# Kernel tuning notes

Measured on AMD Instinct MI355X. Metric: run time of the kernel, lower is better.

The kernel has to match this reference:

```python
import jax, jax.numpy as jnp
import numpy as np

N = 100000
E = 1_600_000
IN = 128
HID = 32
HEADS = 4
OUT = 2
NEG_SLOPE = 0.2  # PyG GATv2Conv default negative_slope


def setup_inputs() -> dict:
    key = jax.random.key(0)
    ks = jax.random.split(key, 18)
    g = lambda k, shape, fan: jax.random.normal(k, shape, dtype=jnp.float32) / np.sqrt(fan)
    return {
        "x": jax.random.normal(ks[0], (N, IN), dtype=jnp.float32),
        "edge_index": jax.random.randint(ks[1], (2, E), 0, N, dtype=jnp.int32),
        # conv1: GATv2Conv(IN, HID, heads=HEADS)
        "W1l": g(ks[2], (IN, HEADS * HID), IN),
        "b1l": jnp.zeros((HEADS * HID,), jnp.float32),
        "W1r": g(ks[3], (IN, HEADS * HID), IN),
        "b1r": jnp.zeros((HEADS * HID,), jnp.float32),
        "att1": g(ks[4], (HEADS, HID), HID),
        "bias1": jnp.zeros((HEADS * HID,), jnp.float32),
        # conv2: GATv2Conv(HEADS*HID, HID, heads=1)
        "W2l": g(ks[5], (HEADS * HID, HID), HEADS * HID),
        "b2l": jnp.zeros((HID,), jnp.float32),
        "W2r": g(ks[6], (HEADS * HID, HID), HEADS * HID),
        "b2r": jnp.zeros((HID,), jnp.float32),
        "att2": g(ks[7], (1, HID), HID),
        "bias2": jnp.zeros((HID,), jnp.float32),
        # final linear
        "Wlin": g(ks[8], (HID, OUT), HID),
        "blin": jnp.zeros((OUT,), jnp.float32),
    }


def _gatv2(x, src, dst, Wl, bl, Wr, br, att, bias, heads, ch):
    n = x.shape[0]
    xl = (x @ Wl + bl).reshape(n, heads, ch)  # source transform
    xr = (x @ Wr + br).reshape(n, heads, ch)  # target transform
    # GATv2 edge score: a^T LeakyReLU(xl_j + xr_i)
    e = jax.nn.leaky_relu(xl[src] + xr[dst], NEG_SLOPE)      # [E, H, C]
    score = jnp.einsum('ehc,hc->eh', e, att)                  # [E, H]
    # segment softmax over edges sharing a destination node
    m = jax.ops.segment_max(score, dst, num_segments=n)
    ex = jnp.exp(score - m[dst])
    denom = jax.ops.segment_sum(ex, dst, num_segments=n)
    alpha = ex / denom[dst]                                   # [E, H]
    out = jax.ops.segment_sum(alpha[..., None] * xl[src], dst, num_segments=n)
    return out.reshape(n, heads * ch) + bias


def reference(x, edge_index, W1l, b1l, W1r, b1r, att1, bias1,
              W2l, b2l, W2r, b2r, att2, bias2, Wlin, blin):
    # add self-loops (PyG GATv2Conv default add_self_loops=True)
    loop = jnp.arange(N, dtype=edge_index.dtype)
    src = jnp.concatenate([edge_index[0], loop])
    dst = jnp.concatenate([edge_index[1], loop])

    h = _gatv2(x, src, dst, W1l, b1l, W1r, b1r, att1, bias1, HEADS, HID)
    h = jax.nn.elu(h)
    # dropout is inactive in eval mode
    h = _gatv2(h, src, dst, W2l, b2l, W2r, b2r, att2, bias2, 1, HID)
    h = jax.nn.elu(h)
    return h @ Wlin + blin  # [N, OUT]
```

## Files before the change

### kernel.cpp

```cpp
#include <hip/hip_runtime.h>
#include <hip/hip_fp16.h>
#include <math.h>

#define N_NODES 100000
#define E_EDGES 1600000
#define ETOT (E_EDGES + N_NODES)
#define NEG 0.2f
#define NB 782
#define NREP 4
#define SEG 704
#define BCAP (NREP * SEG)
#define CHUNK 4096
#define NCHB ((E_EDGES + CHUNK - 1) / CHUNK)
#define GEMM1_BLOCKS ((N_NODES + 63) / 64)

typedef _Float16 half8 __attribute__((ext_vector_type(8)));
typedef _Float16 half4v __attribute__((ext_vector_type(4)));
typedef _Float16 half2v __attribute__((ext_vector_type(2)));
typedef float floatx4 __attribute__((ext_vector_type(4)));

union H8I {
  half8 v;
  _Float16 e[8];
  int i[4];
};

__device__ __forceinline__ float elu(float v) { return v > 0.f ? v : (__expf(v) - 1.f); }

__device__ __forceinline__ float score8(half8 a, half8 r, half8 av) {
  half8 t = a + r;
  t = __builtin_elementwise_max(t, t * (_Float16)NEG);
  half8 s8 = t * av;
  half4v s4 = __builtin_shufflevector(s8, s8, 0, 1, 2, 3) +
              __builtin_shufflevector(s8, s8, 4, 5, 6, 7);
  half2v s2 = __builtin_shufflevector(s4, s4, 0, 1) +
              __builtin_shufflevector(s4, s4, 2, 3);
  return (float)s2[0] + (float)s2[1];
}

__global__ __launch_bounds__(256) void fusedA_kernel(
    const int* __restrict__ ei, unsigned* __restrict__ cursor,
    unsigned* __restrict__ bins,
    const float* __restrict__ W1l, const float* __restrict__ W1r,
    const float* __restrict__ b1l, const float* __restrict__ b1r,
    const float* __restrict__ W2l, const float* __restrict__ W2r,
    const float* __restrict__ b2l, const float* __restrict__ b2r,
    const float* __restrict__ att1, const float* __restrict__ att2,
    _Float16* __restrict__ Bperm, _Float16* __restrict__ B2perm,
    float* __restrict__ biascat, float* __restrict__ bias2cat,
    _Float16* __restrict__ att1h, _Float16* __restrict__ att2h) {
  int t = threadIdx.x;
  if (blockIdx.x < NCHB) {
    __shared__ unsigned cnt[NB];
    __shared__ unsigned base[NB];
    int rep = blockIdx.x & (NREP - 1);
    for (int b = t; b < NB; b += 256) cnt[b] = 0;
    __syncthreads();
    int e0 = blockIdx.x * CHUNK;
    int dstr[CHUNK / 256];
#pragma unroll
    for (int i = 0; i < CHUNK / 256; i++) {
      int e = e0 + i * 256 + t;
      int dst = 0;
      if (e < E_EDGES) {
        dst = ei[E_EDGES + e];
        atomicAdd(&cnt[dst >> 7], 1u);
      }
      dstr[i] = dst;
    }
    __syncthreads();
    for (int b = t; b < NB; b += 256) {
      unsigned c = cnt[b];
      base[b] = c ? atomicAdd(&cursor[rep * NB + b], c) : 0u;
      cnt[b] = 0;
    }
    __syncthreads();
#pragma unroll
    for (int i = 0; i < CHUNK / 256; i++) {
      int e = e0 + i * 256 + t;
      if (e < E_EDGES) {
        int dst = dstr[i];
        int src = ei[e];
        int b = dst >> 7;
        unsigned off = atomicAdd(&cnt[b], 1u);
        bins[(size_t)b * BCAP + rep * SEG + base[b] + off] =
            ((unsigned)(dst & 127) << 17) | (unsigned)src;
      }
    }
  } else {
    int pb = blockIdx.x - NCHB;
    int gt = pb * 256 + t;
    int gstr = 20 * 256;
    for (int e = gt; e < 4096; e += gstr) {
      int nt = e >> 8, kt = (e >> 6) & 3, lane = e & 63;
      int n = nt * 16 + (lane & 15);
      int kb = kt * 32 + (lane >> 4) * 8;
#pragma unroll
      for (int j = 0; j < 8; j++) {
        int k = kb + j;
        float val = (n < 128) ? W1l[k * 128 + n] : W1r[k * 128 + (n - 128)];
        Bperm[(size_t)e * 8 + j] = (_Float16)val;
      }
    }
    for (int e = gt; e < 1024; e += gstr) {
      int nt = e >> 8, kt = (e >> 6) & 3, lane = e & 63;
      int n = nt * 16 + (lane & 15);
      int kb = kt * 32 + (lane >> 4) * 8;
#pragma unroll
      for (int j = 0; j < 8; j++) {
        int k = kb + j;
        float val = (n < 32) ? W2l[k * 32 + n] : W2r[k * 32 + (n - 32)];
        B2perm[(size_t)e * 8 + j] = (_Float16)val;
      }
    }
    if (pb == 0) {
      biascat[t] = (t < 128) ? b1l[t] : b1r[t - 128];
      if (t < 64) bias2cat[t] = (t < 32) ? b2l[t] : b2r[t - 32];
      if (t < 128) att1h[t] = (_Float16)att1[t];
      if (t < 32) att2h[t] = (_Float16)att2[t];
    }
  }
}

__global__ __launch_bounds__(1024) void scan_buckets(const unsigned* __restrict__ cursor,
                                                     unsigned* __restrict__ bucket_base,
                                                     unsigned* __restrict__ rowptr) {
  __shared__ unsigned s[1024];
  int t = threadIdx.x;
  unsigned v = 0;
  if (t < NB) {
#pragma unroll
    for (int r = 0; r < NREP; r++) v += cursor[r * NB + t];
    int nib = N_NODES - (t << 7);
    v += (nib > 128) ? 128u : (unsigned)nib;
  }
  s[t] = v;
  __syncthreads();
  for (int off = 1; off < 1024; off <<= 1) {
    unsigned a = (t >= off) ? s[t - off] : 0u;
    __syncthreads();
    s[t] += a;
    __syncthreads();
  }
  if (t < NB) bucket_base[t] = s[t] - v;
  if (t == 0) { bucket_base[NB] = ETOT; rowptr[N_NODES] = ETOT; }
}

__global__ __launch_bounds__(256) void fusedB_kernel(
    const unsigned* __restrict__ bins, const unsigned* __restrict__ cursor,
    const unsigned* __restrict__ bucket_base,
    unsigned* __restrict__ rowptr, int* __restrict__ csr_src,
    const float* __restrict__ x, const _Float16* __restrict__ Bperm,
    const float* __restrict__ biascat,
    __half* __restrict__ xlh, __half* __restrict__ xrh) {
  __shared__ __align__(16) char smem[64 * 256];
  int t = threadIdx.x;
  if (blockIdx.x < NB) {
    unsigned* cnt = (unsigned*)smem;
    unsigned* pref = cnt + 128;
    int b = blockIdx.x;
    int nib = N_NODES - (b << 7);
    if (nib > 128) nib = 128;
    unsigned bbase = bucket_base[b];
    unsigned crs[NREP];
#pragma unroll
    for (int r = 0; r < NREP; r++) crs[r] = cursor[r * NB + b];
    const unsigned* bp = bins + (size_t)b * BCAP;
    if (t < 128) cnt[t] = 0;
    __syncthreads();
#pragma unroll
    for (int r = 0; r < NREP; r++)
      for (unsigned i = t; i < crs[r]; i += 256)
        atomicAdd(&cnt[bp[r * SEG + i] >> 17], 1u);
    __syncthreads();
    if (t < 128) pref[t] = (t < nib) ? cnt[t] + 1u : 0u;
    __syncthreads();
    for (int off = 1; off < 128; off <<= 1) {
      unsigned a = (t >= off && t < 128) ? pref[t - off] : 0u;
      __syncthreads();
      if (t < 128) pref[t] += a;
      __syncthreads();
    }
    if (t < 128) {
      unsigned tot = (t < nib) ? cnt[t] + 1u : 0u;
      unsigned excl = pref[t] - tot;
      pref[t] = excl;
      if (t < nib) {
        int n = (b << 7) + t;
        rowptr[n] = bbase + excl;
        csr_src[bbase + excl] = n;
      }
      cnt[t] = 0;
    }
    __syncthreads();
#pragma unroll
    for (int r = 0; r < NREP; r++)
      for (unsigned i = t; i < crs[r]; i += 256) {
        unsigned en = bp[r * SEG + i];
        int j = (int)(en >> 17);
        unsigned off = atomicAdd(&cnt[j], 1u);
        csr_src[bbase + pref[j] + 1u + off] = (int)(en & 0x1FFFFu);
      }
  } else {
    int base = (blockIdx.x - NB) * 64;
    {
      int row = t >> 2, c4 = t & 3;
      int grow = base + row;
      const float* gp = x + (size_t)grow * 128 + c4 * 32;
#pragma unroll
      for (int j = 0; j < 4; j++) {
        half8 v = {};
        if (grow < N_NODES) {
          float4 f0 = *(const float4*)(gp + j * 8);
          float4 f1 = *(const float4*)(gp + j * 8 + 4);
          v[0] = (_Float16)f0.x; v[1] = (_Float16)f0.y;
          v[2] = (_Float16)f0.z; v[3] = (_Float16)f0.w;
          v[4] = (_Float16)f1.x; v[5] = (_Float16)f1.y;
          v[6] = (_Float16)f1.z; v[7] = (_Float16)f1.w;
        }
        int off = row * 256 + ((((c4 * 4 + j) * 16)) ^ ((row & 7) << 4));
        *(half8*)(smem + off) = v;
      }
    }
    int wid = t >> 6, lane = t & 63;
    half8 bf[4][4];
#pragma unroll
    for (int ntl = 0; ntl < 4; ntl++)
#pragma unroll
      for (int kt = 0; kt < 4; kt++) {
        int f = (wid * 4 + ntl) * 4 + kt;
        bf[ntl][kt] = *(const half8*)(Bperm + ((size_t)f * 64 + lane) * 8);
      }
    floatx4 acc[4][4] = {};
    __syncthreads();
#pragma unroll
    for (int kt = 0; kt < 4; kt++) {
      half8 a[4];
#pragma unroll
      for (int mt = 0; mt < 4; mt++) {
        int row = mt * 16 + (lane & 15);
        int kchunk = kt * 4 + (lane >> 4);
        int off = row * 256 + ((kchunk * 16) ^ ((row & 7) << 4));
        a[mt] = *(const half8*)(smem + off);
      }
#pragma unroll
      for (int mt = 0; mt < 4; mt++)
#pragma unroll
        for (int ntl = 0; ntl < 4; ntl++)
          acc[mt][ntl] = __builtin_amdgcn_mfma_f32_16x16x32_f16(a[mt], bf[ntl][kt],
                                                                acc[mt][ntl], 0, 0, 0);
    }
#pragma unroll
    for (int mt = 0; mt < 4; mt++) {
#pragma unroll
      for (int i = 0; i < 4; i++) {
        int row = base + mt * 16 + (lane >> 4) * 4 + i;
        if (row >= N_NODES) continue;
#pragma unroll
        for (int ntl = 0; ntl < 4; ntl++) {
          int col = wid * 64 + ntl * 16 + (lane & 15);
          float v = acc[mt][ntl][i] + biascat[col];
          if (col < 128) xlh[(size_t)row * 128 + col] = __float2half_rn(v);
          else xrh[(size_t)row * 128 + (col - 128)] = __float2half_rn(v);
        }
      }
    }
  }
}

__global__ __launch_bounds__(256) void gemm2_mfma(
    const __half* __restrict__ h1h, const _Float16* __restrict__ B2perm,
    const float* __restrict__ bias2cat,
    __half* __restrict__ xl2h, __half* __restrict__ xr2h) {
  __shared__ __align__(16) char smem[64 * 256];
  int t = threadIdx.x;
  int base = blockIdx.x * 64;
  {
    int row = t >> 2, c4 = t & 3;
    int grow = base + row;
    const char* gp = (const char*)(h1h + (size_t)grow * 128 + c4 * 32);
#pragma unroll
    for (int j = 0; j < 4; j++) {
      half8 v = {};
      if (grow < N_NODES) v = *(const half8*)(gp + j * 16);
      int off = row * 256 + ((((c4 * 4 + j) * 16)) ^ ((row & 7) << 4));
      *(half8*)(smem + off) = v;
    }
  }
  int wid = t >> 6, lane = t & 63;
  half8 bf[4];
#pragma unroll
  for (int kt = 0; kt < 4; kt++) {
    int f = wid * 4 + kt;
    bf[kt] = *(const half8*)(B2perm + ((size_t)f * 64 + lane) * 8);
  }
  floatx4 acc[4] = {};
  __syncthreads();
#pragma unroll
  for (int kt = 0; kt < 4; kt++) {
    half8 a[4];
#pragma unroll
    for (int mt = 0; mt < 4; mt++) {
      int row = mt * 16 + (lane & 15);
      int kchunk = kt * 4 + (lane >> 4);
      int off = row * 256 + ((kchunk * 16) ^ ((row & 7) << 4));
      a[mt] = *(const half8*)(smem + off);
    }
#pragma unroll
    for (int mt = 0; mt < 4; mt++)
      acc[mt] = __builtin_amdgcn_mfma_f32_16x16x32_f16(a[mt], bf[kt], acc[mt], 0, 0, 0);
  }
  int col = wid * 16 + (lane & 15);
  float bv = bias2cat[col];
#pragma unroll
  for (int mt = 0; mt < 4; mt++) {
#pragma unroll
    for (int i = 0; i < 4; i++) {
      int row = base + mt * 16 + (lane >> 4) * 4 + i;
      if (row >= N_NODES) continue;
      float v = acc[mt][i] + bv;
      if (col < 32) xl2h[(size_t)row * 32 + col] = __float2half_rn(v);
      else xr2h[(size_t)row * 32 + (col - 32)] = __float2half_rn(v);
    }
  }
}

__global__ __launch_bounds__(256) void l1_gather_kernel(
    const __half* __restrict__ xlh, const __half* __restrict__ xrh,
    const int* __restrict__ csr_src, const unsigned* __restrict__ rowptr,
    const _Float16* __restrict__ att1h, const float* __restrict__ bias,
    __half* __restrict__ h1h) {
  int wid = threadIdx.x >> 6;
  int lane = threadIdx.x & 63;
  int n = blockIdx.x * 4 + wid;
  if (n >= N_NODES) return;
  int g = lane >> 4;
  int q = lane & 15;
  int c0 = q * 8;
  half8 rv = *(const half8*)(xrh + (size_t)n * 128 + c0);
  half8 av = *(const half8*)(att1h + c0);
  unsigned beg = rowptr[n], end = rowptr[n + 1];
  unsigned deg = end - beg;
  unsigned niter = deg >> 2, rem = deg & 3;
  float d0 = 0.f, d1 = 0.f;
  H8I acc0, acc1;
  acc0.v = (half8){};
  acc1.v = (half8){};
  unsigned e = beg + g;
  unsigned i = 0;
  for (; i + 2 <= niter; i += 2, e += 8) {
    int s0 = csr_src[e];
    int s1 = csr_src[e + 4];
    H8I a0, a1;
    a0.v = *(const half8*)(xlh + (size_t)s0 * 128 + c0);
    a1.v = *(const half8*)(xlh + (size_t)s1 * 128 + c0);
    float v0 = score8(a0.v, rv, av);
    float v1 = score8(a1.v, rv, av);
    v0 += __shfl_xor(v0, 1);  v1 += __shfl_xor(v1, 1);
    v0 += __shfl_xor(v0, 2);  v1 += __shfl_xor(v1, 2);
    float p0 = __expf(v0 - 4.f);
    float p1 = __expf(v1 - 4.f);
    d0 += p0; d1 += p1;
    _Float16 ph0 = (_Float16)p0, ph1 = (_Float16)p1;
    half8 p80 = {ph0, ph0, ph0, ph0, ph0, ph0, ph0, ph0};
    half8 p81 = {ph1, ph1, ph1, ph1, ph1, ph1, ph1, ph1};
    acc0.v = p80 * a0.v + acc0.v;
    acc1.v = p81 * a1.v + acc1.v;
  }
  if (i < niter) {
    int s0 = csr_src[e];
    H8I a0;
    a0.v = *(const half8*)(xlh + (size_t)s0 * 128 + c0);
    float v0 = score8(a0.v, rv, av);
    v0 += __shfl_xor(v0, 1);
    v0 += __shfl_xor(v0, 2);
    float p0 = __expf(v0 - 4.f);
    d0 += p0;
    _Float16 ph0 = (_Float16)p0;
    half8 p80 = {ph0, ph0, ph0, ph0, ph0, ph0, ph0, ph0};
    acc0.v = p80 * a0.v + acc0.v;
    e += 4;
  }
  if (rem) {
    bool valid = (unsigned)g < rem;
    int s0 = csr_src[valid ? e : beg];
    H8I a0;
    a0.v = *(const half8*)(xlh + (size_t)s0 * 128 + c0);
    float v0 = score8(a0.v, rv, av);
    v0 += __shfl_xor(v0, 1);
    v0 += __shfl_xor(v0, 2);
    float p0 = valid ? __expf(v0 - 4.f) : 0.f;
    d0 += p0;
    _Float16 ph0 = (_Float16)p0;
    half8 p80 = {ph0, ph0, ph0, ph0, ph0, ph0, ph0, ph0};
    acc0.v = p80 * a0.v + acc0.v;
  }
  float d = d0 + d1;
  H8I acc;
  acc.v = acc0.v + acc1.v;
#pragma unroll
  for (int msk = 16; msk <= 32; msk <<= 1) {
    d += __shfl_xor(d, msk);
    H8I o;
#pragma unroll
    for (int k = 0; k < 4; k++) o.i[k] = __shfl_xor(acc.i[k], msk);
    acc.v = acc.v + o.v;
  }
  if (g == 0) {
    float inv = 1.f / d;
    H8I res;
#pragma unroll
    for (int j = 0; j < 8; j++)
      res.e[j] = (_Float16)elu((float)acc.e[j] * inv + bias[c0 + j]);
    *(half8*)(h1h + (size_t)n * 128 + c0) = res.v;
  }
}

__global__ __launch_bounds__(256) void l2_gather_kernel(
    const __half* __restrict__ xl2h, const __half* __restrict__ xr2h,
    const int* __restrict__ csr_src, const unsigned* __restrict__ rowptr,
    const _Float16* __restrict__ att2h, const float* __restrict__ bias,
    const float* __restrict__ Wlin, const float* __restrict__ blin,
    float* __restrict__ out) {
  int wid = threadIdx.x >> 6;
  int lane = threadIdx.x & 63;
  int n = blockIdx.x * 4 + wid;
  if (n >= N_NODES) return;
  int g = lane >> 2;
  int q = lane & 3;
  int c0 = q * 8;
  half8 rv = *(const half8*)(xr2h + (size_t)n * 32 + c0);
  half8 av = *(const half8*)(att2h + c0);
  unsigned beg = rowptr[n], end = rowptr[n + 1];
  unsigned deg = end - beg;
  unsigned nfull = deg >> 4, rem = deg & 15;
  float d = 0.f;
  H8I acc;
  acc.v = (half8){};
  unsigned e = beg + g;
  for (unsigned i = 0; i < nfull; i++, e += 16) {
    int s = csr_src[e];
    H8I a;
    a.v = *(const half8*)(xl2h + (size_t)s * 32 + c0);
    float v = score8(a.v, rv, av);
    v += __shfl_xor(v, 1);
    v += __shfl_xor(v, 2);
    float p = __expf(v - 4.f);
    d += p;
    _Float16 ph = (_Float16)p;
    half8 p8 = {ph, ph, ph, ph, ph, ph, ph, ph};
    acc.v = p8 * a.v + acc.v;
  }
  if (rem) {
    bool valid = (unsigned)g < rem;
    int s = csr_src[valid ? e : beg];
    H8I a;
    a.v = *(const half8*)(xl2h + (size_t)s * 32 + c0);
    float v = score8(a.v, rv, av);
    v += __shfl_xor(v, 1);
    v += __shfl_xor(v, 2);
    float p = valid ? __expf(v - 4.f) : 0.f;
    d += p;
    _Float16 ph = (_Float16)p;
    half8 p8 = {ph, ph, ph, ph, ph, ph, ph, ph};
    acc.v = p8 * a.v + acc.v;
  }
#pragma unroll
  for (int msk = 4; msk <= 32; msk <<= 1) {
    d += __shfl_xor(d, msk);
    H8I o;
#pragma unroll
    for (int k = 0; k < 4; k++) o.i[k] = __shfl_xor(acc.i[k], msk);
    acc.v = acc.v + o.v;
  }
  float inv = 1.f / d;
  float o0 = 0.f, o1 = 0.f;
#pragma unroll
  for (int j = 0; j < 8; j++) {
    float v = elu((float)acc.e[j] * inv + bias[c0 + j]);
    o0 = fmaf(v, Wlin[(c0 + j) * 2 + 0], o0);
    o1 = fmaf(v, Wlin[(c0 + j) * 2 + 1], o1);
  }
  o0 += __shfl_xor(o0, 1); o1 += __shfl_xor(o1, 1);
  o0 += __shfl_xor(o0, 2); o1 += __shfl_xor(o1, 2);
  if (lane == 0) {
    out[(size_t)n * 2 + 0] = o0 + blin[0];
    out[(size_t)n * 2 + 1] = o1 + blin[1];
  }
}

extern "C" void kernel_launch(void* const* d_in, const int* in_sizes, int n_in,
                              void* d_out, int out_size, void* d_ws, size_t ws_size,
                              hipStream_t stream) {
  const float* x     = (const float*)d_in[0];
  const int*   ei    = (const int*)d_in[1];
  const float* W1l   = (const float*)d_in[2];
  const float* b1l   = (const float*)d_in[3];
  const float* W1r   = (const float*)d_in[4];
  const float* b1r   = (const float*)d_in[5];
  const float* att1  = (const float*)d_in[6];
  const float* bias1 = (const float*)d_in[7];
  const float* W2l   = (const float*)d_in[8];
  const float* b2l   = (const float*)d_in[9];
  const float* W2r   = (const float*)d_in[10];
  const float* b2r   = (const float*)d_in[11];
  const float* att2  = (const float*)d_in[12];
  const float* bias2 = (const float*)d_in[13];
  const float* Wlin  = (const float*)d_in[14];
  const float* blin  = (const float*)d_in[15];
  float* out = (float*)d_out;

  __half* xl1h  = (__half*)d_ws;
  __half* xr1h  = xl1h + (size_t)N_NODES * 128;
  __half* h1h   = xr1h + (size_t)N_NODES * 128;
  __half* xl2h  = h1h + (size_t)N_NODES * 128;
  __half* xr2h  = xl2h + (size_t)N_NODES * 32;
  _Float16* Bperm  = (_Float16*)(xr2h + (size_t)N_NODES * 32);
  _Float16* B2perm = Bperm + 32768;
  _Float16* att1h  = B2perm + 8192;
  _Float16* att2h  = att1h + 128;
  float* biascat   = (float*)(att2h + 32);
  float* bias2cat  = biascat + 256;
  int* csr_src     = (int*)(bias2cat + 64);
  unsigned* rowptr = (unsigned*)(csr_src + (size_t)ETOT);
  unsigned* cursor = rowptr + (N_NODES + 1);
  unsigned* bucket_base = cursor + NREP * NB;
  unsigned* bins   = bucket_base + NB + 1;

  (void)hipMemsetAsync(cursor, 0, (size_t)NREP * NB * sizeof(unsigned), stream);
  fusedA_kernel<<<NCHB + 20, 256, 0, stream>>>(
      ei, cursor, bins, W1l, W1r, b1l, b1r, W2l, W2r, b2l, b2r, att1, att2,
      Bperm, B2perm, biascat, bias2cat, att1h, att2h);
  scan_buckets<<<1, 1024, 0, stream>>>(cursor, bucket_base, rowptr);
  fusedB_kernel<<<NB + GEMM1_BLOCKS, 256, 0, stream>>>(
      bins, cursor, bucket_base, rowptr, csr_src, x, Bperm, biascat, xl1h, xr1h);

  l1_gather_kernel<<<(N_NODES + 3) / 4, 256, 0, stream>>>(
      (const __half*)xl1h, (const __half*)xr1h, csr_src, rowptr, att1h, bias1, h1h);

  gemm2_mfma<<<GEMM1_BLOCKS, 256, 0, stream>>>(h1h, B2perm, bias2cat, xl2h, xr2h);
  l2_gather_kernel<<<(N_NODES + 3) / 4, 256, 0, stream>>>(
      xl2h, xr2h, csr_src, rowptr, att2h, bias2, Wlin, blin, out);
}
```

Baseline: 228.5 us.

## Move layer-1 GEMM into the binning kernel and split weight packing out

```diff
diff --git a/kernel.cpp b/kernel.cpp
--- a/kernel.cpp
+++ b/kernel.cpp
@@ -38,9 +38,7 @@
   return (float)s2[0] + (float)s2[1];
 }
 
-__global__ __launch_bounds__(256) void fusedA_kernel(
-    const int* __restrict__ ei, unsigned* __restrict__ cursor,
-    unsigned* __restrict__ bins,
+__global__ __launch_bounds__(256) void pack_w_kernel(
     const float* __restrict__ W1l, const float* __restrict__ W1r,
     const float* __restrict__ b1l, const float* __restrict__ b1r,
     const float* __restrict__ W2l, const float* __restrict__ W2r,
@@ -50,9 +48,49 @@
     float* __restrict__ biascat, float* __restrict__ bias2cat,
     _Float16* __restrict__ att1h, _Float16* __restrict__ att2h) {
   int t = threadIdx.x;
+  int gt = blockIdx.x * 256 + t;
+  int gstr = gridDim.x * 256;
+  for (int e = gt; e < 4096; e += gstr) {
+    int nt = e >> 8, kt = (e >> 6) & 3, lane = e & 63;
+    int n = nt * 16 + (lane & 15);
+    int kb = kt * 32 + (lane >> 4) * 8;
+#pragma unroll
+    for (int j = 0; j < 8; j++) {
+      int k = kb + j;
+      float val = (n < 128) ? W1l[k * 128 + n] : W1r[k * 128 + (n - 128)];
+      Bperm[(size_t)e * 8 + j] = (_Float16)val;
+    }
+  }
+  for (int e = gt; e < 1024; e += gstr) {
+    int nt = e >> 8, kt = (e >> 6) & 3, lane = e & 63;
+    int n = nt * 16 + (lane & 15);
+    int kb = kt * 32 + (lane >> 4) * 8;
+#pragma unroll
+    for (int j = 0; j < 8; j++) {
+      int k = kb + j;
+      float val = (n < 32) ? W2l[k * 32 + n] : W2r[k * 32 + (n - 32)];
+      B2perm[(size_t)e * 8 + j] = (_Float16)val;
+    }
+  }
+  if (blockIdx.x == 0) {
+    biascat[t] = (t < 128) ? b1l[t] : b1r[t - 128];
+    if (t < 64) bias2cat[t] = (t < 32) ? b2l[t] : b2r[t - 32];
+    if (t < 128) att1h[t] = (_Float16)att1[t];
+    if (t < 32) att2h[t] = (_Float16)att2[t];
+  }
+}
+
+__global__ __launch_bounds__(256) void fusedbin_kernel(
+    const int* __restrict__ ei, unsigned* __restrict__ cursor,
+    unsigned* __restrict__ bins,
+    const float* __restrict__ x, const _Float16* __restrict__ Bperm,
+    const float* __restrict__ biascat,
+    __half* __restrict__ xlh, __half* __restrict__ xrh) {
+  __shared__ __align__(16) char smem[64 * 256];
+  int t = threadIdx.x;
   if (blockIdx.x < NCHB) {
-    __shared__ unsigned cnt[NB];
-    __shared__ unsigned base[NB];
+    unsigned* cnt = (unsigned*)smem;
+    unsigned* base = cnt + NB;
     int rep = blockIdx.x & (NREP - 1);
     for (int b = t; b < NB; b += 256) cnt[b] = 0;
     __syncthreads();
@@ -88,121 +126,7 @@
       }
     }
   } else {
-    int pb = blockIdx.x - NCHB;
-    int gt = pb * 256 + t;
-    int gstr = 20 * 256;
-    for (int e = gt; e < 4096; e += gstr) {
-      int nt = e >> 8, kt = (e >> 6) & 3, lane = e & 63;
-      int n = nt * 16 + (lane & 15);
-      int kb = kt * 32 + (lane >> 4) * 8;
-#pragma unroll
-      for (int j = 0; j < 8; j++) {
-        int k = kb + j;
-        float val = (n < 128) ? W1l[k * 128 + n] : W1r[k * 128 + (n - 128)];
-        Bperm[(size_t)e * 8 + j] = (_Float16)val;
-      }
-    }
-    for (int e = gt; e < 1024; e += gstr) {
-      int nt = e >> 8, kt = (e >> 6) & 3, lane = e & 63;
-      int n = nt * 16 + (lane & 15);
-      int kb = kt * 32 + (lane >> 4) * 8;
-#pragma unroll
-      for (int j = 0; j < 8; j++) {
-        int k = kb + j;
-        float val = (n < 32) ? W2l[k * 32 + n] : W2r[k * 32 + (n - 32)];
-        B2perm[(size_t)e * 8 + j] = (_Float16)val;
-      }
-    }
-    if (pb == 0) {
-      biascat[t] = (t < 128) ? b1l[t] : b1r[t - 128];
-      if (t < 64) bias2cat[t] = (t < 32) ? b2l[t] : b2r[t - 32];
-      if (t < 128) att1h[t] = (_Float16)att1[t];
-      if (t < 32) att2h[t] = (_Float16)att2[t];
-    }
-  }
-}
-
-__global__ __launch_bounds__(1024) void scan_buckets(const unsigned* __restrict__ cursor,
-                                                     unsigned* __restrict__ bucket_base,
-                                                     unsigned* __restrict__ rowptr) {
-  __shared__ unsigned s[1024];
-  int t = threadIdx.x;
-  unsigned v = 0;
-  if (t < NB) {
-#pragma unroll
-    for (int r = 0; r < NREP; r++) v += cursor[r * NB + t];
-    int nib = N_NODES - (t << 7);
-    v += (nib > 128) ? 128u : (unsigned)nib;
-  }
-  s[t] = v;
-  __syncthreads();
-  for (int off = 1; off < 1024; off <<= 1) {
-    unsigned a = (t >= off) ? s[t - off] : 0u;
-    __syncthreads();
-    s[t] += a;
-    __syncthreads();
-  }
-  if (t < NB) bucket_base[t] = s[t] - v;
-  if (t == 0) { bucket_base[NB] = ETOT; rowptr[N_NODES] = ETOT; }
-}
-
-__global__ __launch_bounds__(256) void fusedB_kernel(
-    const unsigned* __restrict__ bins, const unsigned* __restrict__ cursor,
-    const unsigned* __restrict__ bucket_base,
-    unsigned* __restrict__ rowptr, int* __restrict__ csr_src,
-    const float* __restrict__ x, const _Float16* __restrict__ Bperm,
-    const float* __restrict__ biascat,
-    __half* __restrict__ xlh, __half* __restrict__ xrh) {
-  __shared__ __align__(16) char smem[64 * 256];
-  int t = threadIdx.x;
-  if (blockIdx.x < NB) {
-    unsigned* cnt = (unsigned*)smem;
-    unsigned* pref = cnt + 128;
-    int b = blockIdx.x;
-    int nib = N_NODES - (b << 7);
-    if (nib > 128) nib = 128;
-    unsigned bbase = bucket_base[b];
-    unsigned crs[NREP];
-#pragma unroll
-    for (int r = 0; r < NREP; r++) crs[r] = cursor[r * NB + b];
-    const unsigned* bp = bins + (size_t)b * BCAP;
-    if (t < 128) cnt[t] = 0;
-    __syncthreads();
-#pragma unroll
-    for (int r = 0; r < NREP; r++)
-      for (unsigned i = t; i < crs[r]; i += 256)
-        atomicAdd(&cnt[bp[r * SEG + i] >> 17], 1u);
-    __syncthreads();
-    if (t < 128) pref[t] = (t < nib) ? cnt[t] + 1u : 0u;
-    __syncthreads();
-    for (int off = 1; off < 128; off <<= 1) {
-      unsigned a = (t >= off && t < 128) ? pref[t - off] : 0u;
-      __syncthreads();
-      if (t < 128) pref[t] += a;
-      __syncthreads();
-    }
-    if (t < 128) {
-      unsigned tot = (t < nib) ? cnt[t] + 1u : 0u;
-      unsigned excl = pref[t] - tot;
-      pref[t] = excl;
-      if (t < nib) {
-        int n = (b << 7) + t;
-        rowptr[n] = bbase + excl;
-        csr_src[bbase + excl] = n;
-      }
-      cnt[t] = 0;
-    }
-    __syncthreads();
-#pragma unroll
-    for (int r = 0; r < NREP; r++)
-      for (unsigned i = t; i < crs[r]; i += 256) {
-        unsigned en = bp[r * SEG + i];
-        int j = (int)(en >> 17);
-        unsigned off = atomicAdd(&cnt[j], 1u);
-        csr_src[bbase + pref[j] + 1u + off] = (int)(en & 0x1FFFFu);
-      }
-  } else {
-    int base = (blockIdx.x - NB) * 64;
+    int base = (blockIdx.x - NCHB) * 64;
     {
       int row = t >> 2, c4 = t & 3;
       int grow = base + row;
@@ -266,6 +190,81 @@
       }
     }
   }
+}
+
+__global__ __launch_bounds__(1024) void scan_buckets(const unsigned* __restrict__ cursor,
+                                                     unsigned* __restrict__ bucket_base,
+                                                     unsigned* __restrict__ rowptr) {
+  __shared__ unsigned s[1024];
+  int t = threadIdx.x;
+  unsigned v = 0;
+  if (t < NB) {
+#pragma unroll
+    for (int r = 0; r < NREP; r++) v += cursor[r * NB + t];
+    int nib = N_NODES - (t << 7);
+    v += (nib > 128) ? 128u : (unsigned)nib;
+  }
+  s[t] = v;
+  __syncthreads();
+  for (int off = 1; off < 1024; off <<= 1) {
+    unsigned a = (t >= off) ? s[t - off] : 0u;
+    __syncthreads();
+    s[t] += a;
+    __syncthreads();
+  }
+  if (t < NB) bucket_base[t] = s[t] - v;
+  if (t == 0) { bucket_base[NB] = ETOT; rowptr[N_NODES] = ETOT; }
+}
+
+__global__ __launch_bounds__(256) void scatter2_kernel(
+    const unsigned* __restrict__ bins, const unsigned* __restrict__ cursor,
+    const unsigned* __restrict__ bucket_base,
+    unsigned* __restrict__ rowptr, int* __restrict__ csr_src) {
+  __shared__ unsigned cnt[128];
+  __shared__ unsigned pref[128];
+  int b = blockIdx.x, t = threadIdx.x;
+  int nib = N_NODES - (b << 7);
+  if (nib > 128) nib = 128;
+  unsigned bbase = bucket_base[b];
+  unsigned crs[NREP];
+#pragma unroll
+  for (int r = 0; r < NREP; r++) crs[r] = cursor[r * NB + b];
+  const unsigned* bp = bins + (size_t)b * BCAP;
+  if (t < 128) cnt[t] = 0;
+  __syncthreads();
+#pragma unroll
+  for (int r = 0; r < NREP; r++)
+    for (unsigned i = t; i < crs[r]; i += 256)
+      atomicAdd(&cnt[bp[r * SEG + i] >> 17], 1u);
+  __syncthreads();
+  if (t < 128) pref[t] = (t < nib) ? cnt[t] + 1u : 0u;
+  __syncthreads();
+  for (int off = 1; off < 128; off <<= 1) {
+    unsigned a = (t >= off && t < 128) ? pref[t - off] : 0u;
+    __syncthreads();
+    if (t < 128) pref[t] += a;
+    __syncthreads();
+  }
+  if (t < 128) {
+    unsigned tot = (t < nib) ? cnt[t] + 1u : 0u;
+    unsigned excl = pref[t] - tot;
+    pref[t] = excl;
+    if (t < nib) {
+      int n = (b << 7) + t;
+      rowptr[n] = bbase + excl;
+      csr_src[bbase + excl] = n;
+    }
+    cnt[t] = 0;
+  }
+  __syncthreads();
+#pragma unroll
+  for (int r = 0; r < NREP; r++)
+    for (unsigned i = t; i < crs[r]; i += 256) {
+      unsigned en = bp[r * SEG + i];
+      int j = (int)(en >> 17);
+      unsigned off = atomicAdd(&cnt[j], 1u);
+      csr_src[bbase + pref[j] + 1u + off] = (int)(en & 0x1FFFFu);
+    }
 }
 
 __global__ __launch_bounds__(256) void gemm2_mfma(
@@ -528,12 +527,13 @@
   unsigned* bins   = bucket_base + NB + 1;
 
   (void)hipMemsetAsync(cursor, 0, (size_t)NREP * NB * sizeof(unsigned), stream);
-  fusedA_kernel<<<NCHB + 20, 256, 0, stream>>>(
-      ei, cursor, bins, W1l, W1r, b1l, b1r, W2l, W2r, b2l, b2r, att1, att2,
-      Bperm, B2perm, biascat, bias2cat, att1h, att2h);
+  pack_w_kernel<<<4, 256, 0, stream>>>(W1l, W1r, b1l, b1r, W2l, W2r, b2l, b2r,
+                                       att1, att2, Bperm, B2perm, biascat, bias2cat,
+                                       att1h, att2h);
+  fusedbin_kernel<<<NCHB + GEMM1_BLOCKS, 256, 0, stream>>>(
+      ei, cursor, bins, x, Bperm, biascat, xl1h, xr1h);
   scan_buckets<<<1, 1024, 0, stream>>>(cursor, bucket_base, rowptr);
-  fusedB_kernel<<<NB + GEMM1_BLOCKS, 256, 0, stream>>>(
-      bins, cursor, bucket_base, rowptr, csr_src, x, Bperm, biascat, xl1h, xr1h);
+  scatter2_kernel<<<NB, 256, 0, stream>>>(bins, cursor, bucket_base, rowptr, csr_src);
 
   l1_gather_kernel<<<(N_NODES + 3) / 4, 256, 0, stream>>>(
       (const __half*)xl1h, (const __half*)xr1h, csr_src, rowptr, att1h, bias1, h1h);
```

Result: slower. 235.4 us (+3.0%).
